# Kernel optimization log

Measured on AMD Instinct MI355X. Metric: run time of the kernel, lower is better.

The kernel has to match this reference:

```python
import jax, jax.numpy as jnp
import numpy as np
import math

H = 256  # hidden dim hardcoded in module; d_k = 256
EPS = 1e-5  # torch LayerNorm eps


def _mlp2(x, W1, b1, W2, b2):
    # nn.Sequential(Linear, Tanh, Linear, Tanh)
    return jnp.tanh(jnp.tanh(x @ W1 + b1) @ W2 + b2)


def _ln(x, w, b):
    mu = x.mean(-1, keepdims=True)
    var = ((x - mu) ** 2).mean(-1, keepdims=True)
    return (x - mu) / jnp.sqrt(var + EPS) * w + b


def setup_inputs():
    B, N, D, A = 128, 32, 128, 16
    key = jax.random.key(0)
    ks = jax.random.split(key, 32)

    def lin(k, i, o):
        return jax.random.normal(k, (i, o), jnp.float32) / np.sqrt(i).astype(np.float32)

    inp = {
        'states': jax.random.normal(ks[0], (B, N, D), jnp.float32),
        'policies': jax.nn.softmax(jax.random.normal(ks[1], (B, N, A), jnp.float32), axis=-1),
        'actions': jax.nn.one_hot(jax.random.randint(ks[2], (B, N), 0, A), A, dtype=jnp.float32),
    }
    # two-layer MLP params: state_embed(se), key(k), query(q), state_act_embed(sa),
    # attention_value(av), curr_agent_state_embed(ca)
    ins = {'se': D, 'k': H, 'q': H, 'sa': D + A, 'av': H, 'ca': D}
    i = 3
    for n in ['se', 'k', 'q', 'sa', 'av', 'ca']:
        inp[n + '_W1'] = lin(ks[i], ins[n], H); inp[n + '_b1'] = jnp.zeros((H,), jnp.float32)
        inp[n + '_W2'] = lin(ks[i + 1], H, H);  inp[n + '_b2'] = jnp.zeros((H,), jnp.float32)
        i += 2
    inp['f_W1'] = lin(ks[i], 2 * H, H); inp['f_b1'] = jnp.zeros((H,), jnp.float32); i += 1
    inp['f_W2'] = lin(ks[i], H, H);     inp['f_b2'] = jnp.zeros((H,), jnp.float32); i += 1
    inp['f_W3'] = lin(ks[i], H, A);     inp['f_b3'] = jnp.zeros((A,), jnp.float32); i += 1
    inp['ln1_w'] = jnp.ones((H,), jnp.float32); inp['ln1_b'] = jnp.zeros((H,), jnp.float32)
    inp['ln2_w'] = jnp.ones((H,), jnp.float32); inp['ln2_b'] = jnp.zeros((H,), jnp.float32)
    return inp


def reference(states, policies, actions,
              se_W1, se_b1, se_W2, se_b2,
              k_W1, k_b1, k_W2, k_b2,
              q_W1, q_b1, q_W2, q_b2,
              sa_W1, sa_b1, sa_W2, sa_b2,
              av_W1, av_b1, av_W2, av_b2,
              ca_W1, ca_b1, ca_W2, ca_b2,
              f_W1, f_b1, f_W2, f_b2, f_W3, f_b3,
              ln1_w, ln1_b, ln2_w, ln2_b):
    B, N, D = states.shape
    # remove_self_loops: per-agent gather of all other agents (static index map)
    nbr = np.array([[j for j in range(N) if j != i] for i in range(N)])  # [N, N-1]
    states_key = states[:, nbr, :]        # [B,N,N-1,D]
    actions_nb = actions[:, nbr, :]       # [B,N,N-1,A]
    obs_actions = jnp.concatenate([states_key, actions_nb], axis=-1)

    sq_embed = _mlp2(states, se_W1, se_b1, se_W2, se_b2)       # [B,N,256] (query path)
    sk_embed = _mlp2(states_key, se_W1, se_b1, se_W2, se_b2)   # [B,N,N-1,256]
    key_obs = _mlp2(sk_embed, k_W1, k_b1, k_W2, k_b2)          # [B,N,N-1,256]
    query_obs = _mlp2(sq_embed, q_W1, q_b1, q_W2, q_b2)        # [B,N,256]

    scores = jnp.einsum('bnd,bnmd->bnm', query_obs, key_obs) / math.sqrt(float(H))
    weight = jax.nn.softmax(scores, axis=-1)                   # [B,N,N-1]

    # weight_assignment: insert 1.0 at the self position
    rows = np.arange(N)[:, None]
    weights_full = jnp.zeros((B, N, N), weight.dtype).at[:, rows, nbr].set(weight)
    weights_full = weights_full.at[:, np.arange(N), np.arange(N)].set(1.0)

    oa_embed = _mlp2(obs_actions, sa_W1, sa_b1, sa_W2, sa_b2)  # [B,N,N-1,256]
    att_vals = _mlp2(oa_embed, av_W1, av_b1, av_W2, av_b2)     # [B,N,N-1,256]
    node_feat = jnp.einsum('bnm,bnmd->bnd', weight, att_vals)  # [B,N,256]
    node_feat = _ln(oa_embed.mean(axis=-2) + node_feat, ln1_w, ln1_b)

    cur = _mlp2(states, ca_W1, ca_b1, ca_W2, ca_b2)
    cur = _ln(cur + sk_embed.mean(axis=-2) + sq_embed, ln2_w, ln2_b)

    feat = jnp.concatenate([cur, node_feat], axis=-1)          # [B,N,512]
    h = jnp.tanh(feat @ f_W1 + f_b1)
    h = jnp.tanh(h @ f_W2 + f_b2)
    Q = h @ f_W3 + f_b3                                        # [B,N,A]

    Value = jnp.einsum('bna,bma->bnm', Q, policies)            # Q @ policies^T -> [B,N,N]
    Q_value = jnp.sum(actions * Q, axis=-1, keepdims=True)     # [B,N,1]
    return Value, Q_value, weights_full
```

## Files before the change

kernel.cpp:

```cpp
#include <hip/hip_runtime.h>
#include <hip/hip_bf16.h>


struct Ptrs37 { const void* p[37]; };
struct Meta37 { int sz[37]; unsigned off[37]; };
struct PrepW  { int widx[14]; unsigned dstOff[14]; int K[14]; int Kp[14]; };

typedef __attribute__((ext_vector_type(8))) short bf16x8;
typedef __attribute__((ext_vector_type(4))) float f32x4;

__device__ __forceinline__ bool is_bf16_env(const void* ln1w) {
  return (*(const unsigned int*)ln1w) != 0x3f800000u;
}
__device__ __forceinline__ unsigned short f2bf(float f) {
  union { __hip_bfloat16 h; unsigned short u; } cv;
  cv.h = __float2bfloat16(f);
  return cv.u;
}

__global__ __launch_bounds__(256) void prep_all_kernel(Ptrs37 P, Meta37 M, PrepW pw,
                                                       float* __restrict__ F,
                                                       unsigned short* __restrict__ WT,
                                                       float* __restrict__ OAin) {
  bool bf = is_bf16_env(P.p[33]);
  int y = blockIdx.y;
  int stride = gridDim.x * 256;
  int g0 = blockIdx.x * 256 + threadIdx.x;
  if (y < 37) {
    int n = M.sz[y];
    float* dst = F + M.off[y];
    if (bf) {
      const unsigned short* s = (const unsigned short*)P.p[y];
      for (int idx = g0; idx < n; idx += stride)
        dst[idx] = __uint_as_float(((unsigned int)s[idx]) << 16);
    } else {
      const float* s = (const float*)P.p[y];
      for (int idx = g0; idx < n; idx += stride) dst[idx] = s[idx];
    }
  } else if (y < 51) {
    int t = y - 37;
    const void* src = P.p[pw.widx[t]];
    unsigned short* dst = WT + pw.dstOff[t];
    int K = pw.K[t], Kp = pw.Kp[t];
    int total = 256 * Kp;
    for (int idx = g0; idx < total; idx += stride) {
      int n = idx / Kp, k = idx - n * Kp;
      unsigned short v = 0;
      if (k < K) {
        size_t si = (size_t)k * 256 + n;
        v = bf ? ((const unsigned short*)src)[si] : f2bf(((const float*)src)[si]);
      }
      dst[idx] = v;
    }
  } else {
    const void* S = P.p[0];
    const void* A = P.p[2];
    for (int gid = g0; gid < 4096 * 160; gid += stride) {
      int r = gid / 160, c = gid - r * 160;
      float v = 0.f;
      if (c < 128) {
        size_t si = (size_t)r * 128 + c;
        v = bf ? __uint_as_float(((unsigned int)((const unsigned short*)S)[si]) << 16)
               : ((const float*)S)[si];
      } else if (c < 144) {
        size_t si = (size_t)r * 16 + (c - 128);
        v = bf ? __uint_as_float(((unsigned int)((const unsigned short*)A)[si]) << 16)
               : ((const float*)A)[si];
      }
      OAin[gid] = v;
    }
  }
}

struct GemmDesc { const float* X; const unsigned short* WT; const float* bias; float* Y; int K; };
struct GemmStage { GemmDesc g[3]; };

__global__ __launch_bounds__(256) void gemm_mfma_kernel(GemmStage st) {
  GemmDesc d = st.g[blockIdx.z];
  const float* __restrict__ X = d.X;
  const unsigned short* __restrict__ WT = d.WT;
  const float* __restrict__ Bv = d.bias;
  float* __restrict__ Y = d.Y;
  const int K = d.K;
  __shared__ uint4 AsB[2][256];
  __shared__ uint4 BsB[2][256];
  const int tid = threadIdx.x;
  const int l = tid & 63, w = tid >> 6;
  const int m0 = blockIdx.y << 6, n0 = blockIdx.x << 6;
  const int wm = w >> 1, wn = w & 1;
  const int arow = wm * 32 + (l & 15);
  const int brow = wn * 32 + (l & 15);
  const int koff = (l >> 4) * 8;
  const float* ax = X + (size_t)(m0 + (tid >> 2)) * K + (tid & 3) * 8;
  const unsigned short* bg = WT + (size_t)(n0 + (tid >> 2)) * K + (tid & 3) * 8;
  f32x4 acc[2][2] = {};
  {
    float4 t0 = *(const float4*)ax;
    float4 t1 = *(const float4*)(ax + 4);
    uint4 bv = *(const uint4*)bg;
    unsigned short as8[8];
    as8[0] = f2bf(t0.x); as8[1] = f2bf(t0.y); as8[2] = f2bf(t0.z); as8[3] = f2bf(t0.w);
    as8[4] = f2bf(t1.x); as8[5] = f2bf(t1.y); as8[6] = f2bf(t1.z); as8[7] = f2bf(t1.w);
    AsB[0][tid] = *(const uint4*)as8;
    BsB[0][tid] = bv;
  }
  __syncthreads();
  int cur = 0;
  for (int k0 = 0; k0 < K; k0 += 32) {
    const bool more = (k0 + 32) < K;
    float4 n0f, n1f; uint4 nb;
    if (more) {
      n0f = *(const float4*)(ax + k0 + 32);
      n1f = *(const float4*)(ax + k0 + 36);
      nb  = *(const uint4*)(bg + k0 + 32);
    }
    const char* Ab = (const char*)AsB[cur];
    const char* Bb = (const char*)BsB[cur];
    bf16x8 a0 = *(const bf16x8*)(Ab + arow * 64 + koff * 2);
    bf16x8 a1 = *(const bf16x8*)(Ab + (arow + 16) * 64 + koff * 2);
    bf16x8 b0 = *(const bf16x8*)(Bb + brow * 64 + koff * 2);
    bf16x8 b1 = *(const bf16x8*)(Bb + (brow + 16) * 64 + koff * 2);
    acc[0][0] = __builtin_amdgcn_mfma_f32_16x16x32_bf16(a0, b0, acc[0][0], 0, 0, 0);
    acc[0][1] = __builtin_amdgcn_mfma_f32_16x16x32_bf16(a0, b1, acc[0][1], 0, 0, 0);
    acc[1][0] = __builtin_amdgcn_mfma_f32_16x16x32_bf16(a1, b0, acc[1][0], 0, 0, 0);
    acc[1][1] = __builtin_amdgcn_mfma_f32_16x16x32_bf16(a1, b1, acc[1][1], 0, 0, 0);
    if (more) {
      unsigned short as8[8];
      as8[0] = f2bf(n0f.x); as8[1] = f2bf(n0f.y); as8[2] = f2bf(n0f.z); as8[3] = f2bf(n0f.w);
      as8[4] = f2bf(n1f.x); as8[5] = f2bf(n1f.y); as8[6] = f2bf(n1f.z); as8[7] = f2bf(n1f.w);
      AsB[cur ^ 1][tid] = *(const uint4*)as8;
      BsB[cur ^ 1][tid] = nb;
      __syncthreads();
      cur ^= 1;
    }
  }
  const int col0 = n0 + wn * 32 + (l & 15);
  const int rbase = m0 + wm * 32 + (l >> 4) * 4;
#pragma unroll
  for (int ni = 0; ni < 2; ++ni) {
    int col = col0 + ni * 16;
    float bias = Bv[col];
#pragma unroll
    for (int mi = 0; mi < 2; ++mi) {
#pragma unroll
      for (int r = 0; r < 4; ++r) {
        int row = rbase + mi * 16 + r;
        Y[(size_t)row * 256 + col] = tanhf(acc[mi][ni][r] + bias);
      }
    }
  }
}

__global__ __launch_bounds__(256) void attn_kernel(
    const float* __restrict__ Qb, const float* __restrict__ Kb,
    const float* __restrict__ AVp, const float* __restrict__ OAp,
    const float* __restrict__ SEp,
    float* __restrict__ NF, float* __restrict__ sumOA, float* __restrict__ sumSE,
    void* __restrict__ dout, const void* __restrict__ ln1w) {
  const size_t WF_OFF = 135168;
  int b = blockIdx.x;
  int tid = threadIdx.x;
  bool bf = is_bf16_env(ln1w);
  __shared__ float AVs[32 * 260];
  __shared__ float wsT[32][36];

  const float* avg = AVp + (size_t)b * 8192;
  for (int i = tid * 4; i < 8192; i += 1024) {
    int j = i >> 8, c = i & 255;
    *(float4*)&AVs[j * 260 + c] = *(const float4*)(avg + i);
  }
  {
    int c = tid;
    float sa = 0.f, ss = 0.f;
    const float* oab = OAp + (size_t)b * 8192 + c;
    const float* seb = SEp + (size_t)b * 8192 + c;
#pragma unroll 4
    for (int j = 0; j < 32; ++j) { sa += oab[j * 256]; ss += seb[j * 256]; }
    sumOA[b * 256 + c] = sa;
    sumSE[b * 256 + c] = ss;
  }

  int l = tid & 63, w = tid >> 6;
  int j = l & 31, h = l >> 5;
  const float* kbase = Kb + (size_t)b * 8192 + j * 256 + h * 128;
  const float* qbase = Qb + (size_t)b * 8192 + h * 128;
  for (int q = 0; q < 2; ++q) {
    int n0 = w * 8 + q * 4;
    float acc0 = 0.f, acc1 = 0.f, acc2 = 0.f, acc3 = 0.f;
    for (int t = 0; t < 32; ++t) {
      float4 kv = *(const float4*)(kbase + t * 4);
      float4 q0 = *(const float4*)(qbase + (n0 + 0) * 256 + t * 4);
      float4 q1 = *(const float4*)(qbase + (n0 + 1) * 256 + t * 4);
      float4 q2 = *(const float4*)(qbase + (n0 + 2) * 256 + t * 4);
      float4 q3 = *(const float4*)(qbase + (n0 + 3) * 256 + t * 4);
      acc0 += q0.x * kv.x + q0.y * kv.y + q0.z * kv.z + q0.w * kv.w;
      acc1 += q1.x * kv.x + q1.y * kv.y + q1.z * kv.z + q1.w * kv.w;
      acc2 += q2.x * kv.x + q2.y * kv.y + q2.z * kv.z + q2.w * kv.w;
      acc3 += q3.x * kv.x + q3.y * kv.y + q3.z * kv.z + q3.w * kv.w;
    }
#pragma unroll
    for (int i = 0; i < 4; ++i) {
      float part = (i == 0) ? acc0 : (i == 1) ? acc1 : (i == 2) ? acc2 : acc3;
      float full = part + __shfl_down(part, 32);
      int n = n0 + i;
      float sc = full * 0.0625f;
      if (j == n) sc = -1e30f;
      float mx = sc;
      mx = fmaxf(mx, __shfl_xor(mx, 16));
      mx = fmaxf(mx, __shfl_xor(mx, 8));
      mx = fmaxf(mx, __shfl_xor(mx, 4));
      mx = fmaxf(mx, __shfl_xor(mx, 2));
      mx = fmaxf(mx, __shfl_xor(mx, 1));
      float e = __expf(sc - mx);
      float s = e;
      s += __shfl_xor(s, 16); s += __shfl_xor(s, 8); s += __shfl_xor(s, 4);
      s += __shfl_xor(s, 2);  s += __shfl_xor(s, 1);
      float wgt = e / s;
      if (l < 32) {
        wsT[j][n] = wgt;
        size_t oi = WF_OFF + ((size_t)(b * 32 + n)) * 32 + j;
        float ov = (j == n) ? 1.0f : wgt;
        if (bf) ((__hip_bfloat16*)dout)[oi] = __float2bfloat16(ov);
        else    ((float*)dout)[oi] = ov;
      }
    }
  }
  __syncthreads();

  int tx = tid & 63, tyy = tid >> 6;
  float accn[8][4] = {};
  for (int jj = 0; jj < 32; ++jj) {
    float4 av = *(const float4*)&AVs[jj * 260 + (tx << 2)];
    const float* wr = &wsT[jj][tyy * 8];
#pragma unroll
    for (int g = 0; g < 8; ++g) {
      float wv = wr[g];
      accn[g][0] += av.x * wv; accn[g][1] += av.y * wv;
      accn[g][2] += av.z * wv; accn[g][3] += av.w * wv;
    }
  }
#pragma unroll
  for (int g = 0; g < 8; ++g) {
    float4 o = make_float4(accn[g][0], accn[g][1], accn[g][2], accn[g][3]);
    *(float4*)&NF[((size_t)(b * 32 + tyy * 8 + g)) * 256 + (tx << 2)] = o;
  }
}

__global__ __launch_bounds__(64) void ln_kernel(
    const float* __restrict__ NF, const float* __restrict__ sOA, const float* __restrict__ OAp,
    const float* __restrict__ Cc, const float* __restrict__ sSE, const float* __restrict__ SEp,
    const float* __restrict__ w1, const float* __restrict__ b1,
    const float* __restrict__ w2, const float* __restrict__ b2,
    float* __restrict__ feat) {
  int row = blockIdx.x, b = row >> 5, l = threadIdx.x;
  float x[4], y[4];
#pragma unroll
  for (int i = 0; i < 4; ++i) {
    int c = l + (i << 6);
    float oa = OAp[row * 256 + c];
    float se = SEp[row * 256 + c];
    x[i] = NF[row * 256 + c] + (sOA[b * 256 + c] - oa) * (1.0f / 31.0f);
    y[i] = Cc[row * 256 + c] + (sSE[b * 256 + c] - se) * (1.0f / 31.0f) + se;
  }
  float sx = x[0] + x[1] + x[2] + x[3];
  float sy = y[0] + y[1] + y[2] + y[3];
  for (int d = 1; d < 64; d <<= 1) { sx += __shfl_xor(sx, d); sy += __shfl_xor(sy, d); }
  float mx = sx * (1.0f / 256.0f), my = sy * (1.0f / 256.0f);
  float vx = 0.f, vy = 0.f;
#pragma unroll
  for (int i = 0; i < 4; ++i) {
    float dx = x[i] - mx; vx += dx * dx;
    float dy = y[i] - my; vy += dy * dy;
  }
  for (int d = 1; d < 64; d <<= 1) { vx += __shfl_xor(vx, d); vy += __shfl_xor(vy, d); }
  float rx = rsqrtf(vx * (1.0f / 256.0f) + 1e-5f);
  float ry = rsqrtf(vy * (1.0f / 256.0f) + 1e-5f);
#pragma unroll
  for (int i = 0; i < 4; ++i) {
    int c = l + (i << 6);
    feat[(size_t)row * 512 + 256 + c] = (x[i] - mx) * rx * w1[c] + b1[c];
    feat[(size_t)row * 512 + c]       = (y[i] - my) * ry * w2[c] + b2[c];
  }
}

__global__ __launch_bounds__(256) void qfinal_kernel(const float* __restrict__ H2,
                                                     const float* __restrict__ W3,
                                                     const float* __restrict__ b3,
                                                     const float* __restrict__ POL,
                                                     const float* __restrict__ ACT,
                                                     void* __restrict__ dout,
                                                     const void* __restrict__ ln1w) {
  bool bf = is_bf16_env(ln1w);
  int b = blockIdx.x, tid = threadIdx.x;
  __shared__ float h2s[32 * 256];
  __shared__ float w3s[256 * 16];
  __shared__ float qfs[512], pols[512], acts[512];
  {
    const float4* src = (const float4*)(H2 + (size_t)b * 8192);
    float4* dst = (float4*)h2s;
#pragma unroll
    for (int i = 0; i < 8; ++i) dst[tid + i * 256] = src[tid + i * 256];
    const float4* wsrc = (const float4*)W3;
    float4* wdst = (float4*)w3s;
#pragma unroll
    for (int i = 0; i < 4; ++i) wdst[tid + i * 256] = wsrc[tid + i * 256];
  }
  for (int i = tid; i < 512; i += 256) {
    pols[i] = POL[(size_t)b * 512 + i];
    acts[i] = ACT[(size_t)b * 512 + i];
  }
  __syncthreads();
#pragma unroll
  for (int t = 0; t < 2; ++t) {
    int p = tid + t * 256;
    int row = p >> 4, a = p & 15;
    float acc = b3[a];
#pragma unroll 8
    for (int k = 0; k < 256; ++k) acc += h2s[row * 256 + k] * w3s[k * 16 + a];
    qfs[p] = acc;
  }
  __syncthreads();
#pragma unroll
  for (int r = 0; r < 4; ++r) {
    int p = tid + (r << 8);
    int n = p >> 5, m = p & 31;
    float acc = 0.f;
#pragma unroll
    for (int a = 0; a < 16; ++a) acc += qfs[n * 16 + a] * pols[m * 16 + a];
    size_t oi = (size_t)b * 1024 + p;
    if (bf) ((__hip_bfloat16*)dout)[oi] = __float2bfloat16(acc);
    else    ((float*)dout)[oi] = acc;
  }
  if (tid < 32) {
    float acc = 0.f;
#pragma unroll
    for (int a = 0; a < 16; ++a) acc += acts[tid * 16 + a] * qfs[tid * 16 + a];
    size_t oi = 131072 + (size_t)b * 32 + tid;
    if (bf) ((__hip_bfloat16*)dout)[oi] = __float2bfloat16(acc);
    else    ((float*)dout)[oi] = acc;
  }
}

extern "C" void kernel_launch(void* const* d_in, const int* in_sizes, int n_in,
                              void* d_out, int out_size, void* d_ws, size_t ws_size,
                              hipStream_t stream) {
  (void)n_in; (void)out_size; (void)ws_size;
  Ptrs37 P; Meta37 M;
  unsigned off = 0;
  for (int i = 0; i < 37; ++i) {
    P.p[i] = d_in[i];
    M.sz[i] = in_sizes[i];
    M.off[i] = off;
    off += (unsigned)in_sizes[i];
  }
  float* F = (float*)d_ws;
  const unsigned MEG = 1048576u;
  unsigned X0 = (off + 511u) & ~511u;
  float* SE   = F + X0 + 0 * MEG;
  float* QB   = F + X0 + 1 * MEG;
  float* KB   = F + X0 + 2 * MEG;
  float* OA   = F + X0 + 3 * MEG;
  float* AV   = F + X0 + 4 * MEG;
  float* CC   = F + X0 + 5 * MEG;
  float* T1   = F + X0 + 6 * MEG;
  float* T2   = F + X0 + 7 * MEG;
  float* T3   = F + X0 + 8 * MEG;
  float* NF   = F + X0 + 9 * MEG;
  float* FEAT = F + X0 + 10 * MEG;
  float* OAIN = F + X0 + 12 * MEG;
  float* H1   = F + X0 + 13 * MEG;
  float* H2   = F + X0 + 14 * MEG;
  float* SOA  = F + X0 + 15 * MEG;
  float* SSE  = SOA + 32768;
  unsigned short* WT = (unsigned short*)(F + X0 + 16 * MEG);
  auto Wp = [&](int i) { return F + M.off[i]; };
  const void* ln1w_raw = d_in[33];
  const float* ST = F + M.off[0];

  static const int wIdx[14] = {3,5,7,9,11,13,15,17,19,21,23,25,27,29};
  PrepW pw{};
  unsigned wtOff[37] = {};
  int Kp_[37] = {};
  unsigned cum = 0;
  for (int t = 0; t < 14; ++t) {
    int i = wIdx[t];
    int K = in_sizes[i] / 256;
    int Kp = (K + 31) & ~31;
    pw.widx[t] = i;
    pw.dstOff[t] = cum;
    pw.K[t] = K; pw.Kp[t] = Kp;
    wtOff[i] = cum; Kp_[i] = Kp;
    cum += (unsigned)(256 * Kp);
  }

  prep_all_kernel<<<dim3(64, 52), 256, 0, stream>>>(P, M, pw, F, WT, OAIN);

  auto G = [&](const float* X, int wi, int bi, float* Y) {
    GemmDesc g; g.X = X; g.WT = WT + wtOff[wi]; g.bias = Wp(bi); g.Y = Y; g.K = Kp_[wi];
    return g;
  };
  dim3 gg3(4, 64, 3), gg1(4, 64, 1);
  GemmStage s1{{ G(ST, 3, 4, T1),  G(OAIN, 15, 16, T2), G(ST, 23, 24, T3) }};
  gemm_mfma_kernel<<<gg3, 256, 0, stream>>>(s1);
  GemmStage s2{{ G(T1, 5, 6, SE),  G(T2, 17, 18, OA),  G(T3, 25, 26, CC) }};
  gemm_mfma_kernel<<<gg3, 256, 0, stream>>>(s2);
  GemmStage s3{{ G(SE, 7, 8, T1),  G(SE, 11, 12, T2),  G(OA, 19, 20, T3) }};
  gemm_mfma_kernel<<<gg3, 256, 0, stream>>>(s3);
  GemmStage s4{{ G(T1, 9, 10, KB), G(T2, 13, 14, QB), G(T3, 21, 22, AV) }};
  gemm_mfma_kernel<<<gg3, 256, 0, stream>>>(s4);

  attn_kernel<<<128, 256, 0, stream>>>(QB, KB, AV, OA, SE, NF, SOA, SSE, d_out, ln1w_raw);
  ln_kernel<<<4096, 64, 0, stream>>>(NF, SOA, OA, CC, SSE, SE,
                                     Wp(33), Wp(34), Wp(35), Wp(36), FEAT);

  GemmDesc g5 = G(FEAT, 27, 28, H1);
  GemmStage s5{{ g5, g5, g5 }};
  gemm_mfma_kernel<<<gg1, 256, 0, stream>>>(s5);
  GemmDesc g6 = G(H1, 29, 30, H2);
  GemmStage s6{{ g6, g6, g6 }};
  gemm_mfma_kernel<<<gg1, 256, 0, stream>>>(s6);

  qfinal_kernel<<<128, 256, 0, stream>>>(H2, Wp(31), Wp(32),
                                         F + M.off[1], F + M.off[2], d_out, ln1w_raw);
}
```

Baseline: 256.1 us.

## Restructure GEMM so each block computes full-width rows with weights staged in LDS

The MFMA GEMM changes from 64x64 output tiles to 32-row blocks that each compute all 256 output columns. Weight chunks of up to 96 K-columns are staged in shared memory, while activation rows are read straight from global memory into registers and converted to bf16. This reads each activation row only once instead of once per column tile, but every block now loads the whole weight matrix. It also halves the number of blocks per stage and drops the double-buffered pipelining, so load latency is no longer overlapped with MFMA work.

New measurement: 341.3 us. 1.33x slower.

```diff
diff --git a/kernel.cpp b/kernel.cpp
--- a/kernel.cpp
+++ b/kernel.cpp
@@ -76,75 +76,64 @@
 struct GemmStage { GemmDesc g[3]; };
 
 __global__ __launch_bounds__(256) void gemm_mfma_kernel(GemmStage st) {
-  GemmDesc d = st.g[blockIdx.z];
+  GemmDesc d = st.g[blockIdx.y];
   const float* __restrict__ X = d.X;
   const unsigned short* __restrict__ WT = d.WT;
+  const int K = d.K;
+  __shared__ char Ws[256 * 208];
+  const int tid = threadIdx.x;
+  const int l = tid & 63, w = tid >> 6;
+  const int lane16 = l & 15, quad = l >> 4;
+  const int m0 = blockIdx.x << 5;
+  const float* aptr0 = X + (size_t)(m0 + lane16) * K + quad * 8;
+  const float* aptr1 = aptr0 + (size_t)16 * K;
+  f32x4 acc[2][4] = {};
+  for (int kc2 = 0; kc2 < K; kc2 += 96) {
+    const int kc = min(96, K - kc2);
+    const int rowb = kc * 2 + 16;
+    const int chunks = kc >> 3;
+    __syncthreads();
+    for (int i = tid; i < 256 * chunks; i += 256) {
+      int r = i / chunks, c = i - r * chunks;
+      *(uint4*)(Ws + r * rowb + c * 16) =
+          *(const uint4*)(WT + (size_t)r * K + kc2 + c * 8);
+    }
+    __syncthreads();
+    for (int k0 = 0; k0 < kc; k0 += 32) {
+      const int kk = kc2 + k0;
+      bf16x8 a0, a1;
+      {
+        float4 t0 = *(const float4*)(aptr0 + kk);
+        float4 t1 = *(const float4*)(aptr0 + kk + 4);
+        unsigned short u[8] = {f2bf(t0.x), f2bf(t0.y), f2bf(t0.z), f2bf(t0.w),
+                               f2bf(t1.x), f2bf(t1.y), f2bf(t1.z), f2bf(t1.w)};
+        a0 = *(const bf16x8*)u;
+        float4 s0 = *(const float4*)(aptr1 + kk);
+        float4 s1 = *(const float4*)(aptr1 + kk + 4);
+        unsigned short v[8] = {f2bf(s0.x), f2bf(s0.y), f2bf(s0.z), f2bf(s0.w),
+                               f2bf(s1.x), f2bf(s1.y), f2bf(s1.z), f2bf(s1.w)};
+        a1 = *(const bf16x8*)v;
+      }
+#pragma unroll
+      for (int ni = 0; ni < 4; ++ni) {
+        int cc = (w << 6) + ni * 16 + lane16;
+        bf16x8 b = *(const bf16x8*)(Ws + cc * rowb + k0 * 2 + quad * 16);
+        acc[0][ni] = __builtin_amdgcn_mfma_f32_16x16x32_bf16(a0, b, acc[0][ni], 0, 0, 0);
+        acc[1][ni] = __builtin_amdgcn_mfma_f32_16x16x32_bf16(a1, b, acc[1][ni], 0, 0, 0);
+      }
+    }
+  }
   const float* __restrict__ Bv = d.bias;
   float* __restrict__ Y = d.Y;
-  const int K = d.K;
-  __shared__ uint4 AsB[2][256];
-  __shared__ uint4 BsB[2][256];
-  const int tid = threadIdx.x;
-  const int l = tid & 63, w = tid >> 6;
-  const int m0 = blockIdx.y << 6, n0 = blockIdx.x << 6;
-  const int wm = w >> 1, wn = w & 1;
-  const int arow = wm * 32 + (l & 15);
-  const int brow = wn * 32 + (l & 15);
-  const int koff = (l >> 4) * 8;
-  const float* ax = X + (size_t)(m0 + (tid >> 2)) * K + (tid & 3) * 8;
-  const unsigned short* bg = WT + (size_t)(n0 + (tid >> 2)) * K + (tid & 3) * 8;
-  f32x4 acc[2][2] = {};
-  {
-    float4 t0 = *(const float4*)ax;
-    float4 t1 = *(const float4*)(ax + 4);
-    uint4 bv = *(const uint4*)bg;
-    unsigned short as8[8];
-    as8[0] = f2bf(t0.x); as8[1] = f2bf(t0.y); as8[2] = f2bf(t0.z); as8[3] = f2bf(t0.w);
-    as8[4] = f2bf(t1.x); as8[5] = f2bf(t1.y); as8[6] = f2bf(t1.z); as8[7] = f2bf(t1.w);
-    AsB[0][tid] = *(const uint4*)as8;
-    BsB[0][tid] = bv;
-  }
-  __syncthreads();
-  int cur = 0;
-  for (int k0 = 0; k0 < K; k0 += 32) {
-    const bool more = (k0 + 32) < K;
-    float4 n0f, n1f; uint4 nb;
-    if (more) {
-      n0f = *(const float4*)(ax + k0 + 32);
-      n1f = *(const float4*)(ax + k0 + 36);
-      nb  = *(const uint4*)(bg + k0 + 32);
-    }
-    const char* Ab = (const char*)AsB[cur];
-    const char* Bb = (const char*)BsB[cur];
-    bf16x8 a0 = *(const bf16x8*)(Ab + arow * 64 + koff * 2);
-    bf16x8 a1 = *(const bf16x8*)(Ab + (arow + 16) * 64 + koff * 2);
-    bf16x8 b0 = *(const bf16x8*)(Bb + brow * 64 + koff * 2);
-    bf16x8 b1 = *(const bf16x8*)(Bb + (brow + 16) * 64 + koff * 2);
-    acc[0][0] = __builtin_amdgcn_mfma_f32_16x16x32_bf16(a0, b0, acc[0][0], 0, 0, 0);
-    acc[0][1] = __builtin_amdgcn_mfma_f32_16x16x32_bf16(a0, b1, acc[0][1], 0, 0, 0);
-    acc[1][0] = __builtin_amdgcn_mfma_f32_16x16x32_bf16(a1, b0, acc[1][0], 0, 0, 0);
-    acc[1][1] = __builtin_amdgcn_mfma_f32_16x16x32_bf16(a1, b1, acc[1][1], 0, 0, 0);
-    if (more) {
-      unsigned short as8[8];
-      as8[0] = f2bf(n0f.x); as8[1] = f2bf(n0f.y); as8[2] = f2bf(n0f.z); as8[3] = f2bf(n0f.w);
-      as8[4] = f2bf(n1f.x); as8[5] = f2bf(n1f.y); as8[6] = f2bf(n1f.z); as8[7] = f2bf(n1f.w);
-      AsB[cur ^ 1][tid] = *(const uint4*)as8;
-      BsB[cur ^ 1][tid] = nb;
-      __syncthreads();
-      cur ^= 1;
-    }
-  }
-  const int col0 = n0 + wn * 32 + (l & 15);
-  const int rbase = m0 + wm * 32 + (l >> 4) * 4;
-#pragma unroll
-  for (int ni = 0; ni < 2; ++ni) {
-    int col = col0 + ni * 16;
+#pragma unroll
+  for (int ni = 0; ni < 4; ++ni) {
+    int col = (w << 6) + ni * 16 + lane16;
     float bias = Bv[col];
 #pragma unroll
     for (int mi = 0; mi < 2; ++mi) {
 #pragma unroll
       for (int r = 0; r < 4; ++r) {
-        int row = rbase + mi * 16 + r;
+        int row = m0 + mi * 16 + quad * 4 + r;
         Y[(size_t)row * 256 + col] = tanhf(acc[mi][ni][r] + bias);
       }
     }
@@ -399,7 +388,7 @@
     GemmDesc g; g.X = X; g.WT = WT + wtOff[wi]; g.bias = Wp(bi); g.Y = Y; g.K = Kp_[wi];
     return g;
   };
-  dim3 gg3(4, 64, 3), gg1(4, 64, 1);
+  dim3 gg3(128, 3), gg1(128, 1);
   GemmStage s1{{ G(ST, 3, 4, T1),  G(OAIN, 15, 16, T2), G(ST, 23, 24, T3) }};
   gemm_mfma_kernel<<<gg3, 256, 0, stream>>>(s1);
   GemmStage s2{{ G(T1, 5, 6, SE),  G(T2, 17, 18, OA),  G(T3, 25, 26, CC) }};
```

## Store intermediate activations as bf16 instead of fp32 across all stages

Applied to the files above, without the earlier changes.

All intermediate activation buffers (MLP outputs, Q/K/V, features, hidden layers) are now written and read as bf16 rather than fp32. GEMM inputs are loaded directly as bf16 with no per-tile conversion, and the states-only GEMMs read from the packed OA input buffer using a leading dimension. This roughly halves memory traffic between kernels and drops conversion work in the GEMM loop. The cost is extra rounding of intermediates, such as Q/K and attention values, before the fp32 consumers.

Result: faster. 237.8 us (-7.1%).

```diff
diff --git a/kernel.cpp b/kernel.cpp
--- a/kernel.cpp
+++ b/kernel.cpp
@@ -17,11 +17,19 @@
   cv.h = __float2bfloat16(f);
   return cv.u;
 }
+__device__ __forceinline__ float bf2f(unsigned short s) {
+  return __uint_as_float(((unsigned int)s) << 16);
+}
+__device__ __forceinline__ float4 ldbf4(const unsigned short* p) {
+  uint2 u = *(const uint2*)p;
+  const unsigned short* s = (const unsigned short*)&u;
+  return make_float4(bf2f(s[0]), bf2f(s[1]), bf2f(s[2]), bf2f(s[3]));
+}
 
 __global__ __launch_bounds__(256) void prep_all_kernel(Ptrs37 P, Meta37 M, PrepW pw,
                                                        float* __restrict__ F,
                                                        unsigned short* __restrict__ WT,
-                                                       float* __restrict__ OAin) {
+                                                       unsigned short* __restrict__ OAin) {
   bool bf = is_bf16_env(P.p[33]);
   int y = blockIdx.y;
   int stride = gridDim.x * 256;
@@ -57,30 +65,29 @@
     const void* A = P.p[2];
     for (int gid = g0; gid < 4096 * 160; gid += stride) {
       int r = gid / 160, c = gid - r * 160;
-      float v = 0.f;
+      unsigned short v = 0;
       if (c < 128) {
         size_t si = (size_t)r * 128 + c;
-        v = bf ? __uint_as_float(((unsigned int)((const unsigned short*)S)[si]) << 16)
-               : ((const float*)S)[si];
+        v = bf ? ((const unsigned short*)S)[si] : f2bf(((const float*)S)[si]);
       } else if (c < 144) {
         size_t si = (size_t)r * 16 + (c - 128);
-        v = bf ? __uint_as_float(((unsigned int)((const unsigned short*)A)[si]) << 16)
-               : ((const float*)A)[si];
+        v = bf ? ((const unsigned short*)A)[si] : f2bf(((const float*)A)[si]);
       }
       OAin[gid] = v;
     }
   }
 }
 
-struct GemmDesc { const float* X; const unsigned short* WT; const float* bias; float* Y; int K; };
+struct GemmDesc {
+  const unsigned short* X; const unsigned short* WT; const float* bias;
+  unsigned short* Y; int K; int ldx;
+};
 struct GemmStage { GemmDesc g[3]; };
 
 __global__ __launch_bounds__(256) void gemm_mfma_kernel(GemmStage st) {
   GemmDesc d = st.g[blockIdx.z];
-  const float* __restrict__ X = d.X;
+  const unsigned short* __restrict__ X = d.X;
   const unsigned short* __restrict__ WT = d.WT;
-  const float* __restrict__ Bv = d.bias;
-  float* __restrict__ Y = d.Y;
   const int K = d.K;
   __shared__ uint4 AsB[2][256];
   __shared__ uint4 BsB[2][256];
@@ -91,28 +98,19 @@
   const int arow = wm * 32 + (l & 15);
   const int brow = wn * 32 + (l & 15);
   const int koff = (l >> 4) * 8;
-  const float* ax = X + (size_t)(m0 + (tid >> 2)) * K + (tid & 3) * 8;
+  const unsigned short* ag = X + (size_t)(m0 + (tid >> 2)) * d.ldx + (tid & 3) * 8;
   const unsigned short* bg = WT + (size_t)(n0 + (tid >> 2)) * K + (tid & 3) * 8;
   f32x4 acc[2][2] = {};
-  {
-    float4 t0 = *(const float4*)ax;
-    float4 t1 = *(const float4*)(ax + 4);
-    uint4 bv = *(const uint4*)bg;
-    unsigned short as8[8];
-    as8[0] = f2bf(t0.x); as8[1] = f2bf(t0.y); as8[2] = f2bf(t0.z); as8[3] = f2bf(t0.w);
-    as8[4] = f2bf(t1.x); as8[5] = f2bf(t1.y); as8[6] = f2bf(t1.z); as8[7] = f2bf(t1.w);
-    AsB[0][tid] = *(const uint4*)as8;
-    BsB[0][tid] = bv;
-  }
+  AsB[0][tid] = *(const uint4*)ag;
+  BsB[0][tid] = *(const uint4*)bg;
   __syncthreads();
   int cur = 0;
   for (int k0 = 0; k0 < K; k0 += 32) {
     const bool more = (k0 + 32) < K;
-    float4 n0f, n1f; uint4 nb;
+    uint4 na, nb;
     if (more) {
-      n0f = *(const float4*)(ax + k0 + 32);
-      n1f = *(const float4*)(ax + k0 + 36);
-      nb  = *(const uint4*)(bg + k0 + 32);
+      na = *(const uint4*)(ag + k0 + 32);
+      nb = *(const uint4*)(bg + k0 + 32);
     }
     const char* Ab = (const char*)AsB[cur];
     const char* Bb = (const char*)BsB[cur];
@@ -125,15 +123,14 @@
     acc[1][0] = __builtin_amdgcn_mfma_f32_16x16x32_bf16(a1, b0, acc[1][0], 0, 0, 0);
     acc[1][1] = __builtin_amdgcn_mfma_f32_16x16x32_bf16(a1, b1, acc[1][1], 0, 0, 0);
     if (more) {
-      unsigned short as8[8];
-      as8[0] = f2bf(n0f.x); as8[1] = f2bf(n0f.y); as8[2] = f2bf(n0f.z); as8[3] = f2bf(n0f.w);
-      as8[4] = f2bf(n1f.x); as8[5] = f2bf(n1f.y); as8[6] = f2bf(n1f.z); as8[7] = f2bf(n1f.w);
-      AsB[cur ^ 1][tid] = *(const uint4*)as8;
+      AsB[cur ^ 1][tid] = na;
       BsB[cur ^ 1][tid] = nb;
       __syncthreads();
       cur ^= 1;
     }
   }
+  const float* __restrict__ Bv = d.bias;
+  __hip_bfloat16* __restrict__ Y = (__hip_bfloat16*)d.Y;
   const int col0 = n0 + wn * 32 + (l & 15);
   const int rbase = m0 + wm * 32 + (l >> 4) * 4;
 #pragma unroll
@@ -145,16 +142,16 @@
 #pragma unroll
       for (int r = 0; r < 4; ++r) {
         int row = rbase + mi * 16 + r;
-        Y[(size_t)row * 256 + col] = tanhf(acc[mi][ni][r] + bias);
+        Y[(size_t)row * 256 + col] = __float2bfloat16(tanhf(acc[mi][ni][r] + bias));
       }
     }
   }
 }
 
 __global__ __launch_bounds__(256) void attn_kernel(
-    const float* __restrict__ Qb, const float* __restrict__ Kb,
-    const float* __restrict__ AVp, const float* __restrict__ OAp,
-    const float* __restrict__ SEp,
+    const unsigned short* __restrict__ Qb, const unsigned short* __restrict__ Kb,
+    const unsigned short* __restrict__ AVp, const unsigned short* __restrict__ OAp,
+    const unsigned short* __restrict__ SEp,
     float* __restrict__ NF, float* __restrict__ sumOA, float* __restrict__ sumSE,
     void* __restrict__ dout, const void* __restrict__ ln1w) {
   const size_t WF_OFF = 135168;
@@ -164,35 +161,35 @@
   __shared__ float AVs[32 * 260];
   __shared__ float wsT[32][36];
 
-  const float* avg = AVp + (size_t)b * 8192;
+  const unsigned short* avg = AVp + (size_t)b * 8192;
   for (int i = tid * 4; i < 8192; i += 1024) {
     int j = i >> 8, c = i & 255;
-    *(float4*)&AVs[j * 260 + c] = *(const float4*)(avg + i);
+    *(float4*)&AVs[j * 260 + c] = ldbf4(avg + i);
   }
   {
     int c = tid;
     float sa = 0.f, ss = 0.f;
-    const float* oab = OAp + (size_t)b * 8192 + c;
-    const float* seb = SEp + (size_t)b * 8192 + c;
+    const unsigned short* oab = OAp + (size_t)b * 8192 + c;
+    const unsigned short* seb = SEp + (size_t)b * 8192 + c;
 #pragma unroll 4
-    for (int j = 0; j < 32; ++j) { sa += oab[j * 256]; ss += seb[j * 256]; }
+    for (int j = 0; j < 32; ++j) { sa += bf2f(oab[j * 256]); ss += bf2f(seb[j * 256]); }
     sumOA[b * 256 + c] = sa;
     sumSE[b * 256 + c] = ss;
   }
 
   int l = tid & 63, w = tid >> 6;
   int j = l & 31, h = l >> 5;
-  const float* kbase = Kb + (size_t)b * 8192 + j * 256 + h * 128;
-  const float* qbase = Qb + (size_t)b * 8192 + h * 128;
+  const unsigned short* kbase = Kb + (size_t)b * 8192 + j * 256 + h * 128;
+  const unsigned short* qbase = Qb + (size_t)b * 8192 + h * 128;
   for (int q = 0; q < 2; ++q) {
     int n0 = w * 8 + q * 4;
     float acc0 = 0.f, acc1 = 0.f, acc2 = 0.f, acc3 = 0.f;
     for (int t = 0; t < 32; ++t) {
-      float4 kv = *(const float4*)(kbase + t * 4);
-      float4 q0 = *(const float4*)(qbase + (n0 + 0) * 256 + t * 4);
-      float4 q1 = *(const float4*)(qbase + (n0 + 1) * 256 + t * 4);
-      float4 q2 = *(const float4*)(qbase + (n0 + 2) * 256 + t * 4);
-      float4 q3 = *(const float4*)(qbase + (n0 + 3) * 256 + t * 4);
+      float4 kv = ldbf4(kbase + t * 4);
+      float4 q0 = ldbf4(qbase + (n0 + 0) * 256 + t * 4);
+      float4 q1 = ldbf4(qbase + (n0 + 1) * 256 + t * 4);
+      float4 q2 = ldbf4(qbase + (n0 + 2) * 256 + t * 4);
+      float4 q3 = ldbf4(qbase + (n0 + 3) * 256 + t * 4);
       acc0 += q0.x * kv.x + q0.y * kv.y + q0.z * kv.z + q0.w * kv.w;
       acc1 += q1.x * kv.x + q1.y * kv.y + q1.z * kv.z + q1.w * kv.w;
       acc2 += q2.x * kv.x + q2.y * kv.y + q2.z * kv.z + q2.w * kv.w;
@@ -247,20 +244,20 @@
 }
 
 __global__ __launch_bounds__(64) void ln_kernel(
-    const float* __restrict__ NF, const float* __restrict__ sOA, const float* __restrict__ OAp,
-    const float* __restrict__ Cc, const float* __restrict__ sSE, const float* __restrict__ SEp,
+    const float* __restrict__ NF, const float* __restrict__ sOA, const unsigned short* __restrict__ OAp,
+    const unsigned short* __restrict__ Cc, const float* __restrict__ sSE, const unsigned short* __restrict__ SEp,
     const float* __restrict__ w1, const float* __restrict__ b1,
     const float* __restrict__ w2, const float* __restrict__ b2,
-    float* __restrict__ feat) {
+    unsigned short* __restrict__ feat) {
   int row = blockIdx.x, b = row >> 5, l = threadIdx.x;
   float x[4], y[4];
 #pragma unroll
   for (int i = 0; i < 4; ++i) {
     int c = l + (i << 6);
-    float oa = OAp[row * 256 + c];
-    float se = SEp[row * 256 + c];
+    float oa = bf2f(OAp[row * 256 + c]);
+    float se = bf2f(SEp[row * 256 + c]);
     x[i] = NF[row * 256 + c] + (sOA[b * 256 + c] - oa) * (1.0f / 31.0f);
-    y[i] = Cc[row * 256 + c] + (sSE[b * 256 + c] - se) * (1.0f / 31.0f) + se;
+    y[i] = bf2f(Cc[row * 256 + c]) + (sSE[b * 256 + c] - se) * (1.0f / 31.0f) + se;
   }
   float sx = x[0] + x[1] + x[2] + x[3];
   float sy = y[0] + y[1] + y[2] + y[3];
@@ -278,12 +275,12 @@
 #pragma unroll
   for (int i = 0; i < 4; ++i) {
     int c = l + (i << 6);
-    feat[(size_t)row * 512 + 256 + c] = (x[i] - mx) * rx * w1[c] + b1[c];
-    feat[(size_t)row * 512 + c]       = (y[i] - my) * ry * w2[c] + b2[c];
-  }
-}
-
-__global__ __launch_bounds__(256) void qfinal_kernel(const float* __restrict__ H2,
+    feat[(size_t)row * 512 + 256 + c] = f2bf((x[i] - mx) * rx * w1[c] + b1[c]);
+    feat[(size_t)row * 512 + c]       = f2bf((y[i] - my) * ry * w2[c] + b2[c]);
+  }
+}
+
+__global__ __launch_bounds__(256) void qfinal_kernel(const unsigned short* __restrict__ H2,
                                                      const float* __restrict__ W3,
                                                      const float* __restrict__ b3,
                                                      const float* __restrict__ POL,
@@ -296,10 +293,15 @@
   __shared__ float w3s[256 * 16];
   __shared__ float qfs[512], pols[512], acts[512];
   {
-    const float4* src = (const float4*)(H2 + (size_t)b * 8192);
-    float4* dst = (float4*)h2s;
-#pragma unroll
-    for (int i = 0; i < 8; ++i) dst[tid + i * 256] = src[tid + i * 256];
+    const unsigned short* src = H2 + (size_t)b * 8192;
+#pragma unroll
+    for (int i = 0; i < 4; ++i) {
+      int base = (tid + i * 256) * 8;
+      uint4 u = *(const uint4*)(src + base);
+      const unsigned short* s = (const unsigned short*)&u;
+#pragma unroll
+      for (int e = 0; e < 8; ++e) h2s[base + e] = bf2f(s[e]);
+    }
     const float4* wsrc = (const float4*)W3;
     float4* wdst = (float4*)w3s;
 #pragma unroll
@@ -356,26 +358,26 @@
   float* F = (float*)d_ws;
   const unsigned MEG = 1048576u;
   unsigned X0 = (off + 511u) & ~511u;
-  float* SE   = F + X0 + 0 * MEG;
-  float* QB   = F + X0 + 1 * MEG;
-  float* KB   = F + X0 + 2 * MEG;
-  float* OA   = F + X0 + 3 * MEG;
-  float* AV   = F + X0 + 4 * MEG;
-  float* CC   = F + X0 + 5 * MEG;
-  float* T1   = F + X0 + 6 * MEG;
-  float* T2   = F + X0 + 7 * MEG;
-  float* T3   = F + X0 + 8 * MEG;
-  float* NF   = F + X0 + 9 * MEG;
-  float* FEAT = F + X0 + 10 * MEG;
-  float* OAIN = F + X0 + 12 * MEG;
-  float* H1   = F + X0 + 13 * MEG;
-  float* H2   = F + X0 + 14 * MEG;
+  auto BUF = [&](int slot) { return (unsigned short*)(F + X0 + slot * MEG); };
+  unsigned short* SE   = BUF(0);
+  unsigned short* QB   = BUF(1);
+  unsigned short* KB   = BUF(2);
+  unsigned short* OA   = BUF(3);
+  unsigned short* AV   = BUF(4);
+  unsigned short* CC   = BUF(5);
+  unsigned short* T1   = BUF(6);
+  unsigned short* T2   = BUF(7);
+  unsigned short* T3   = BUF(8);
+  float*          NF   = F + X0 + 9 * MEG;
+  unsigned short* FEAT = BUF(10);
+  unsigned short* OAIN = BUF(12);
+  unsigned short* H1   = BUF(13);
+  unsigned short* H2   = BUF(14);
   float* SOA  = F + X0 + 15 * MEG;
   float* SSE  = SOA + 32768;
   unsigned short* WT = (unsigned short*)(F + X0 + 16 * MEG);
   auto Wp = [&](int i) { return F + M.off[i]; };
   const void* ln1w_raw = d_in[33];
-  const float* ST = F + M.off[0];
 
   static const int wIdx[14] = {3,5,7,9,11,13,15,17,19,21,23,25,27,29};
   PrepW pw{};
@@ -395,28 +397,29 @@
 
   prep_all_kernel<<<dim3(64, 52), 256, 0, stream>>>(P, M, pw, F, WT, OAIN);
 
-  auto G = [&](const float* X, int wi, int bi, float* Y) {
-    GemmDesc g; g.X = X; g.WT = WT + wtOff[wi]; g.bias = Wp(bi); g.Y = Y; g.K = Kp_[wi];
+  auto G = [&](const unsigned short* X, int ldx, int wi, int bi, unsigned short* Y) {
+    GemmDesc g; g.X = X; g.WT = WT + wtOff[wi]; g.bias = Wp(bi); g.Y = Y;
+    g.K = Kp_[wi]; g.ldx = ldx;
     return g;
   };
   dim3 gg3(4, 64, 3), gg1(4, 64, 1);
-  GemmStage s1{{ G(ST, 3, 4, T1),  G(OAIN, 15, 16, T2), G(ST, 23, 24, T3) }};
+  GemmStage s1{{ G(OAIN, 160, 3, 4, T1),  G(OAIN, 160, 15, 16, T2), G(OAIN, 160, 23, 24, T3) }};
   gemm_mfma_kernel<<<gg3, 256, 0, stream>>>(s1);
-  GemmStage s2{{ G(T1, 5, 6, SE),  G(T2, 17, 18, OA),  G(T3, 25, 26, CC) }};
+  GemmStage s2{{ G(T1, 256, 5, 6, SE),  G(T2, 256, 17, 18, OA),  G(T3, 256, 25, 26, CC) }};
   gemm_mfma_kernel<<<gg3, 256, 0, stream>>>(s2);
-  GemmStage s3{{ G(SE, 7, 8, T1),  G(SE, 11, 12, T2),  G(OA, 19, 20, T3) }};
+  GemmStage s3{{ G(SE, 256, 7, 8, T1),  G(SE, 256, 11, 12, T2),  G(OA, 256, 19, 20, T3) }};
   gemm_mfma_kernel<<<gg3, 256, 0, stream>>>(s3);
-  GemmStage s4{{ G(T1, 9, 10, KB), G(T2, 13, 14, QB), G(T3, 21, 22, AV) }};
+  GemmStage s4{{ G(T1, 256, 9, 10, KB), G(T2, 256, 13, 14, QB), G(T3, 256, 21, 22, AV) }};
   gemm_mfma_kernel<<<gg3, 256, 0, stream>>>(s4);
 
   attn_kernel<<<128, 256, 0, stream>>>(QB, KB, AV, OA, SE, NF, SOA, SSE, d_out, ln1w_raw);
   ln_kernel<<<4096, 64, 0, stream>>>(NF, SOA, OA, CC, SSE, SE,
                                      Wp(33), Wp(34), Wp(35), Wp(36), FEAT);
 
-  GemmDesc g5 = G(FEAT, 27, 28, H1);
+  GemmDesc g5 = G(FEAT, 512, 27, 28, H1);
   GemmStage s5{{ g5, g5, g5 }};
   gemm_mfma_kernel<<<gg1, 256, 0, stream>>>(s5);
-  GemmDesc g6 = G(H1, 29, 30, H2);
+  GemmDesc g6 = G(H1, 256, 29, 30, H2);
   GemmStage s6{{ g6, g6, g6 }};
   gemm_mfma_kernel<<<gg1, 256, 0, stream>>>(s6);
 
```
